# Kernel tuning notes

Measured on AMD Instinct MI355X. Metric: run time of the kernel, lower is better.

Reference implementation:

```python
import jax, jax.numpy as jnp
import numpy as np


def setup_inputs() -> dict:
    key = jax.random.key(0)
    k1, k2, k3 = jax.random.split(key, 3)
    B, C2, H, W = 8, 128, 28, 28   # resnet18 layer2 output for 224x224 input
    C3, H3, W3 = 256, 14, 14       # resnet18 layer3 output
    M = 30000                      # memory bank patches (post-coreset)
    f2 = jax.random.normal(k1, (B, C2, H, W), dtype=jnp.float32)
    f3 = jax.random.normal(k2, (B, C3, H3, W3), dtype=jnp.float32)
    memory_bank = jax.random.normal(k3, (M, C2 + C3), dtype=jnp.float32)
    return {"f2": f2, "f3": f3, "memory_bank": memory_bank}


def reference(f2, f3, memory_bank):
    """PatchCore predict: multi-layer embed + brute-force 1-NN euclidean distance.

    f2: [B,C2,H,W] (layer2 feats), f3: [B,C3,H3,W3] (layer3 feats),
    memory_bank: [M, C2+C3]. Returns (patch_scores [B,H,W], img_scores [B]).
    """
    B, C2, H, W = f2.shape
    C3 = f3.shape[1]
    # F.interpolate(..., mode='bilinear', align_corners=False) == jax.image.resize bilinear
    f3_up = jax.image.resize(f3, (B, C3, H, W), method="bilinear")
    emb = jnp.concatenate([f2, f3_up], axis=1)            # [B,C,H,W], C=C2+C3
    C = C2 + C3
    patches = emb.transpose(0, 2, 3, 1).reshape(-1, C)    # [N,C], N=B*H*W
    x_sq = jnp.sum(patches * patches, axis=-1, keepdims=True)      # [N,1]
    m_sq = jnp.sum(memory_bank * memory_bank, axis=-1)[None, :]    # [1,M]
    d2 = x_sq + m_sq - 2.0 * (patches @ memory_bank.T)             # [N,M]
    dists = jnp.sqrt(jnp.maximum(d2, 1e-12))
    nn_dist = jnp.min(dists, axis=1)                               # 1-NN (n_neighbors=1)
    patch_scores = nn_dist.reshape(B, H, W)
    img_scores = jnp.max(patch_scores.reshape(B, -1), axis=1)
    return patch_scores, img_scores
```

## Files before the change

### kernel.cpp

```cpp
#include <hip/hip_runtime.h>
#include <hip/hip_bf16.h>
#include <stdint.h>

typedef float f32x4 __attribute__((ext_vector_type(4)));
typedef short bf16x8 __attribute__((ext_vector_type(8)));

#define NPATCH 6272
#define CTOT   384
#define MBANK  30000
#define MROWS  6400
#define NCOLS  30208
#define NKT    6

#define NPB    (MROWS / 4)
#define NBB    (NCOLS / 4)

__global__ __launch_bounds__(256) void prep_kernel(
    const float* __restrict__ f2, const float* __restrict__ f3,
    const float* __restrict__ mb,
    __hip_bfloat16* __restrict__ A, __hip_bfloat16* __restrict__ Bb,
    float* __restrict__ x_sq, float* __restrict__ m_sq,
    float* __restrict__ nn_d2)
{
  const int lane = threadIdx.x & 63;
  const int sub  = threadIdx.x >> 6;

  if (blockIdx.x < NPB) {
    const int n = blockIdx.x * 4 + sub;
    if (n >= NPATCH) {
      #pragma unroll
      for (int j = 0; j < 6; ++j) A[(size_t)n * CTOT + j * 64 + lane] = __float2bfloat16(0.f);
      return;
    }
    const int b = n / 784;
    const int hw = n - b * 784;
    const int h = hw / 28;
    const int w = hw - h * 28;

    int h0, h1, w0i, w1i; float wh0, wh1, ww0, ww1;
    if (h & 1) { int k = h >> 1; h0 = k; h1 = (k + 1 < 14) ? k + 1 : 13; wh0 = 0.75f; wh1 = 0.25f; }
    else       { int k = h >> 1; h0 = (k > 0) ? k - 1 : 0; h1 = k;       wh0 = 0.25f; wh1 = 0.75f; }
    if (w & 1) { int k = w >> 1; w0i = k; w1i = (k + 1 < 14) ? k + 1 : 13; ww0 = 0.75f; ww1 = 0.25f; }
    else       { int k = w >> 1; w0i = (k > 0) ? k - 1 : 0; w1i = k;       ww0 = 0.25f; ww1 = 0.75f; }

    float ssum = 0.f;
    #pragma unroll
    for (int j = 0; j < 6; ++j) {
      const int c = j * 64 + lane;
      float v;
      if (j < 2) {
        v = f2[(((size_t)b * 128 + c) * 28 + h) * 28 + w];
      } else {
        const int c3 = c - 128;
        const float* p = f3 + ((size_t)b * 256 + c3) * 196;
        v = wh0 * (ww0 * p[h0 * 14 + w0i] + ww1 * p[h0 * 14 + w1i]) +
            wh1 * (ww0 * p[h1 * 14 + w0i] + ww1 * p[h1 * 14 + w1i]);
      }
      A[(size_t)n * CTOT + c] = __float2bfloat16(v);
      ssum += v * v;
    }
    #pragma unroll
    for (int off = 32; off; off >>= 1) ssum += __shfl_xor(ssum, off);
    if (lane == 0) { x_sq[n] = ssum; nn_d2[n] = __uint_as_float(0x7f800000u); }
  } else {
    const int m = (blockIdx.x - NPB) * 4 + sub;
    if (m < MBANK) {
      float ssum = 0.f;
      #pragma unroll
      for (int j = 0; j < 3; ++j) {
        const int c = j * 128 + lane * 2;
        const float2 v = *(const float2*)&mb[(size_t)m * CTOT + c];
        short2 o;
        o.x = (short)__bfloat16_as_ushort(__float2bfloat16(v.x));
        o.y = (short)__bfloat16_as_ushort(__float2bfloat16(v.y));
        *(short2*)&Bb[(size_t)m * CTOT + c] = o;
        ssum += v.x * v.x + v.y * v.y;
      }
      #pragma unroll
      for (int off = 32; off; off >>= 1) ssum += __shfl_xor(ssum, off);
      if (lane == 0) m_sq[m] = ssum;
    } else {
      #pragma unroll
      for (int j = 0; j < 6; ++j) Bb[(size_t)m * CTOT + j * 64 + lane] = __float2bfloat16(0.f);
      if (lane == 0) m_sq[m] = __uint_as_float(0x7f800000u);
    }
  }
}

__device__ __forceinline__ void gl_lds16(const void* g, void* l) {
  __builtin_amdgcn_global_load_lds(
      (const __attribute__((address_space(1))) uint32_t*)g,
      (__attribute__((address_space(3))) uint32_t*)l, 16, 0, 0);
}

__global__ __launch_bounds__(512, 2) void gemm_min_kernel(
    const __hip_bfloat16* __restrict__ A, const __hip_bfloat16* __restrict__ B,
    const float* __restrict__ x_sq, const float* __restrict__ m_sq,
    float* __restrict__ nn_d2)
{
  __shared__ __align__(16) short As[2][256 * 64];
  __shared__ __align__(16) short Bs[2][256 * 64];
  const int tid  = threadIdx.x;
  const int lane = tid & 63;
  const int wid  = tid >> 6;
  const int wr = wid >> 2;
  const int wc = wid & 3;
  const int row0 = blockIdx.y * 256;
  const int col0 = blockIdx.x * 256;

  f32x4 acc[8][4];
  #pragma unroll
  for (int i = 0; i < 8; ++i)
    #pragma unroll
    for (int j = 0; j < 4; ++j) acc[i][j] = (f32x4){0.f, 0.f, 0.f, 0.f};

  auto stage_pair = [&](int kt, int buf, int j) {
    const int k0 = kt * 64;
    const int cb = j * 512 + wid * 64;
    const int c  = cb + lane;
    const int r  = c >> 3;
    const int ch = (c & 7) ^ (r & 7);
    gl_lds16(A + (size_t)(row0 + r) * CTOT + k0 + ch * 8, &As[buf][cb * 8]);
    gl_lds16(B + (size_t)(col0 + r) * CTOT + k0 + ch * 8, &Bs[buf][cb * 8]);
  };

  #pragma unroll
  for (int j = 0; j < 4; ++j) stage_pair(0, 0, j);
  #pragma unroll
  for (int j = 0; j < 4; ++j) stage_pair(1, 1, j);
  asm volatile("s_waitcnt vmcnt(8)" ::: "memory");
  __builtin_amdgcn_s_barrier();

  const int sw = lane & 7;
  const int rA = wr * 128 + (lane & 15);
  const int rB = wc * 64 + (lane & 15);
  const int kq = lane >> 4;
  const int ch0 = (kq ^ sw) << 4;
  const int ch1 = ((4 + kq) ^ sw) << 4;

  #pragma unroll
  for (int t = 0; t < NKT; ++t) {
    const int cur = t & 1;
    const char* lA = (const char*)As[cur];
    const char* lB = (const char*)Bs[cur];
    const bool st = (t >= 1) && (t + 1 < NKT);
    bf16x8 a0[8], b0[4], a1[8], b1[4];

    #pragma unroll
    for (int ni = 0; ni < 4; ++ni) b0[ni] = *(const bf16x8*)(lB + (rB + ni * 16) * 128 + ch0);
    #pragma unroll
    for (int mi = 0; mi < 4; ++mi) a0[mi] = *(const bf16x8*)(lA + (rA + mi * 16) * 128 + ch0);
    if (st) stage_pair(t + 1, cur ^ 1, 0);
    __builtin_amdgcn_s_barrier();
    asm volatile("s_waitcnt lgkmcnt(0)" ::: "memory");
    __builtin_amdgcn_s_setprio(1);
    #pragma unroll
    for (int mi = 0; mi < 4; ++mi)
      #pragma unroll
      for (int ni = 0; ni < 4; ++ni)
        acc[mi][ni] = __builtin_amdgcn_mfma_f32_16x16x32_bf16(a0[mi], b0[ni], acc[mi][ni], 0, 0, 0);
    __builtin_amdgcn_s_setprio(0);
    __builtin_amdgcn_s_barrier();

    #pragma unroll
    for (int mi = 4; mi < 8; ++mi) a0[mi] = *(const bf16x8*)(lA + (rA + mi * 16) * 128 + ch0);
    if (st) stage_pair(t + 1, cur ^ 1, 1);
    __builtin_amdgcn_s_barrier();
    asm volatile("s_waitcnt lgkmcnt(0)" ::: "memory");
    __builtin_amdgcn_s_setprio(1);
    #pragma unroll
    for (int mi = 4; mi < 8; ++mi)
      #pragma unroll
      for (int ni = 0; ni < 4; ++ni)
        acc[mi][ni] = __builtin_amdgcn_mfma_f32_16x16x32_bf16(a0[mi], b0[ni], acc[mi][ni], 0, 0, 0);
    __builtin_amdgcn_s_setprio(0);
    __builtin_amdgcn_s_barrier();

    #pragma unroll
    for (int ni = 0; ni < 4; ++ni) b1[ni] = *(const bf16x8*)(lB + (rB + ni * 16) * 128 + ch1);
    #pragma unroll
    for (int mi = 0; mi < 4; ++mi) a1[mi] = *(const bf16x8*)(lA + (rA + mi * 16) * 128 + ch1);
    if (st) stage_pair(t + 1, cur ^ 1, 2);
    __builtin_amdgcn_s_barrier();
    asm volatile("s_waitcnt lgkmcnt(0)" ::: "memory");
    __builtin_amdgcn_s_setprio(1);
    #pragma unroll
    for (int mi = 0; mi < 4; ++mi)
      #pragma unroll
      for (int ni = 0; ni < 4; ++ni)
        acc[mi][ni] = __builtin_amdgcn_mfma_f32_16x16x32_bf16(a1[mi], b1[ni], acc[mi][ni], 0, 0, 0);
    __builtin_amdgcn_s_setprio(0);
    __builtin_amdgcn_s_barrier();

    #pragma unroll
    for (int mi = 4; mi < 8; ++mi) a1[mi] = *(const bf16x8*)(lA + (rA + mi * 16) * 128 + ch1);
    if (st) stage_pair(t + 1, cur ^ 1, 3);
    __builtin_amdgcn_s_barrier();
    asm volatile("s_waitcnt lgkmcnt(0)" ::: "memory");
    __builtin_amdgcn_s_setprio(1);
    #pragma unroll
    for (int mi = 4; mi < 8; ++mi)
      #pragma unroll
      for (int ni = 0; ni < 4; ++ni)
        acc[mi][ni] = __builtin_amdgcn_mfma_f32_16x16x32_bf16(a1[mi], b1[ni], acc[mi][ni], 0, 0, 0);
    __builtin_amdgcn_s_setprio(0);
    if (t + 1 < NKT)
      asm volatile("s_waitcnt vmcnt(0)" ::: "memory");
    __builtin_amdgcn_s_barrier();
  }

  float msq[4];
  #pragma unroll
  for (int ni = 0; ni < 4; ++ni) msq[ni] = m_sq[col0 + wc * 64 + ni * 16 + (lane & 15)];

  #pragma unroll
  for (int mi = 0; mi < 8; ++mi) {
    #pragma unroll
    for (int r = 0; r < 4; ++r) {
      float t = msq[0] - 2.f * acc[mi][0][r];
      #pragma unroll
      for (int ni = 1; ni < 4; ++ni) t = fminf(t, msq[ni] - 2.f * acc[mi][ni][r]);
      t = fminf(t, __shfl_xor(t, 1));
      t = fminf(t, __shfl_xor(t, 2));
      t = fminf(t, __shfl_xor(t, 4));
      t = fminf(t, __shfl_xor(t, 8));
      if ((lane & 15) == 0) {
        const int rg = row0 + wr * 128 + mi * 16 + ((lane >> 4) << 2) + r;
        if (rg < NPATCH) {
          const float v = fmaxf(t + x_sq[rg], 0.f);
          atomicMin((unsigned int*)&nn_d2[rg], __float_as_uint(v));
        }
      }
    }
  }
}

__global__ __launch_bounds__(256) void finalize_kernel(
    const float* __restrict__ nn_d2, float* __restrict__ out)
{
  const int b = blockIdx.x;
  const int tid = threadIdx.x;
  __shared__ float red[4];
  float lmax = 0.f;
  for (int i = tid; i < 784; i += 256) {
    const float d2 = nn_d2[b * 784 + i];
    const float s = sqrtf(fmaxf(d2, 1e-12f));
    out[b * 784 + i] = s;
    lmax = fmaxf(lmax, s);
  }
  #pragma unroll
  for (int off = 32; off; off >>= 1) lmax = fmaxf(lmax, __shfl_xor(lmax, off));
  if ((tid & 63) == 0) red[tid >> 6] = lmax;
  __syncthreads();
  if (tid == 0)
    out[6272 + b] = fmaxf(fmaxf(red[0], red[1]), fmaxf(red[2], red[3]));
}

extern "C" void kernel_launch(void* const* d_in, const int* in_sizes, int n_in,
                              void* d_out, int out_size, void* d_ws, size_t ws_size,
                              hipStream_t stream)
{
  const float* f2 = (const float*)d_in[0];
  const float* f3 = (const float*)d_in[1];
  const float* mb = (const float*)d_in[2];
  float* out = (float*)d_out;

  uint8_t* ws = (uint8_t*)d_ws;
  __hip_bfloat16* A  = (__hip_bfloat16*)(ws);
  __hip_bfloat16* Bb = (__hip_bfloat16*)(ws + 4915200);
  float* x_sq  = (float*)(ws + 28114944);
  float* m_sq  = (float*)(ws + 28140544);
  float* nn_d2 = (float*)(ws + 28261376);

  hipLaunchKernelGGL(prep_kernel, dim3(NPB + NBB), dim3(256), 0, stream,
                     f2, f3, mb, A, Bb, x_sq, m_sq, nn_d2);
  hipLaunchKernelGGL(gemm_min_kernel, dim3(NCOLS / 256, MROWS / 256), dim3(512), 0, stream,
                     A, Bb, x_sq, m_sq, nn_d2);
  hipLaunchKernelGGL(finalize_kernel, dim3(8), dim3(256), 0, stream, nn_d2, out);
}
```

Baseline: 468.4 us.

## Loop GEMM over column tiles per block, drop atomics, tile-transpose prep

The GEMM grid shrinks to 10x25 blocks. Each block walks 12 memory-bank column tiles in sequence, keeps a per-row running minimum, and writes partial minima instead of issuing global atomicMin. The prep kernel now transposes f2 and upsamples f3 through shared-memory tiles so reads are coalesced. x_sq is now computed from the bf16 patches in finalize, which also reduces the partials. This removes atomics and the nn_d2 init but gives only 250 blocks, which may underfill the GPU. The finalize kernel now does a per-thread 384-element norm over only 8 blocks, which adds serial work.

Result: faster. 441.8 us (-5.7%).

```diff
diff --git a/kernel.cpp b/kernel.cpp
--- a/kernel.cpp
+++ b/kernel.cpp
@@ -9,61 +9,79 @@
 #define CTOT   384
 #define MBANK  30000
 #define MROWS  6400
-#define NCOLS  30208
-#define NKT    6
-
-#define NPB    (MROWS / 4)
-#define NBB    (NCOLS / 4)
+#define NCOLS  30720
+#define NCT    120
+#define W      12
+#define NCG    10
+
+#define PF2B   16
+#define PF3B   32
+#define PBANKB (NCOLS / 4)
+#define NPREP  (PF2B + PF3B + PBANKB)
 
 __global__ __launch_bounds__(256) void prep_kernel(
     const float* __restrict__ f2, const float* __restrict__ f3,
     const float* __restrict__ mb,
     __hip_bfloat16* __restrict__ A, __hip_bfloat16* __restrict__ Bb,
-    float* __restrict__ x_sq, float* __restrict__ m_sq,
-    float* __restrict__ nn_d2)
+    float* __restrict__ m_sq)
 {
-  const int lane = threadIdx.x & 63;
-  const int sub  = threadIdx.x >> 6;
-
-  if (blockIdx.x < NPB) {
-    const int n = blockIdx.x * 4 + sub;
-    if (n >= NPATCH) {
-      #pragma unroll
-      for (int j = 0; j < 6; ++j) A[(size_t)n * CTOT + j * 64 + lane] = __float2bfloat16(0.f);
-      return;
-    }
-    const int b = n / 784;
-    const int hw = n - b * 784;
-    const int h = hw / 28;
-    const int w = hw - h * 28;
-
-    int h0, h1, w0i, w1i; float wh0, wh1, ww0, ww1;
-    if (h & 1) { int k = h >> 1; h0 = k; h1 = (k + 1 < 14) ? k + 1 : 13; wh0 = 0.75f; wh1 = 0.25f; }
-    else       { int k = h >> 1; h0 = (k > 0) ? k - 1 : 0; h1 = k;       wh0 = 0.25f; wh1 = 0.75f; }
-    if (w & 1) { int k = w >> 1; w0i = k; w1i = (k + 1 < 14) ? k + 1 : 13; ww0 = 0.75f; ww1 = 0.25f; }
-    else       { int k = w >> 1; w0i = (k > 0) ? k - 1 : 0; w1i = k;       ww0 = 0.25f; ww1 = 0.75f; }
-
-    float ssum = 0.f;
-    #pragma unroll
-    for (int j = 0; j < 6; ++j) {
-      const int c = j * 64 + lane;
-      float v;
-      if (j < 2) {
-        v = f2[(((size_t)b * 128 + c) * 28 + h) * 28 + w];
-      } else {
-        const int c3 = c - 128;
-        const float* p = f3 + ((size_t)b * 256 + c3) * 196;
-        v = wh0 * (ww0 * p[h0 * 14 + w0i] + ww1 * p[h0 * 14 + w1i]) +
-            wh1 * (ww0 * p[h1 * 14 + w0i] + ww1 * p[h1 * 14 + w1i]);
-      }
-      A[(size_t)n * CTOT + c] = __float2bfloat16(v);
-      ssum += v * v;
-    }
-    #pragma unroll
-    for (int off = 32; off; off >>= 1) ssum += __shfl_xor(ssum, off);
-    if (lane == 0) { x_sq[n] = ssum; nn_d2[n] = __uint_as_float(0x7f800000u); }
+  __shared__ float tile[64 * 197];
+  const int t = threadIdx.x;
+  const int lane = t & 63;
+  const int grp  = t >> 6;
+
+  if (blockIdx.x < PF2B) {
+    const int b  = blockIdx.x >> 1;
+    const int c0 = (blockIdx.x & 1) * 64;
+    const float* src = f2 + ((size_t)b * 128 + c0) * 784;
+    __hip_bfloat16* dst = A + (size_t)b * 784 * CTOT + c0;
+    for (int hw0 = 0; hw0 < 784; hw0 += 64) {
+      const int nhw = (784 - hw0 < 64) ? (784 - hw0) : 64;
+      __syncthreads();
+      #pragma unroll
+      for (int k = 0; k < 16; ++k) {
+        const int c = grp * 16 + k;
+        if (lane < nhw) tile[c * 65 + lane] = src[(size_t)c * 784 + hw0 + lane];
+      }
+      __syncthreads();
+      #pragma unroll
+      for (int k = 0; k < 16; ++k) {
+        const int r = grp * 16 + k;
+        if (r < nhw) dst[(size_t)(hw0 + r) * CTOT + lane] = __float2bfloat16(tile[lane * 65 + r]);
+      }
+    }
+  } else if (blockIdx.x < PF2B + PF3B) {
+    const int blk = blockIdx.x - PF2B;
+    const int b  = blk >> 2;
+    const int c0 = (blk & 3) * 64;
+    const float* src = f3 + ((size_t)b * 256 + c0) * 196;
+    for (int idx = t; idx < 64 * 196; idx += 256) {
+      const int c = idx / 196, p = idx - c * 196;
+      tile[c * 197 + p] = src[(size_t)c * 196 + p];
+    }
+    __syncthreads();
+    __hip_bfloat16* dst = A + (size_t)b * 784 * CTOT + 128 + c0;
+    for (int hw0 = 0; hw0 < 784; hw0 += 64) {
+      #pragma unroll
+      for (int k = 0; k < 16; ++k) {
+        const int r = grp * 16 + k;
+        const int hw = hw0 + r;
+        if (hw < 784) {
+          const int h = hw / 28, w = hw - h * 28;
+          int h0, h1, w0i, w1i; float wh0, wh1, ww0, ww1;
+          if (h & 1) { int q = h >> 1; h0 = q; h1 = (q + 1 < 14) ? q + 1 : 13; wh0 = 0.75f; wh1 = 0.25f; }
+          else       { int q = h >> 1; h0 = (q > 0) ? q - 1 : 0; h1 = q;       wh0 = 0.25f; wh1 = 0.75f; }
+          if (w & 1) { int q = w >> 1; w0i = q; w1i = (q + 1 < 14) ? q + 1 : 13; ww0 = 0.75f; ww1 = 0.25f; }
+          else       { int q = w >> 1; w0i = (q > 0) ? q - 1 : 0; w1i = q;       ww0 = 0.25f; ww1 = 0.75f; }
+          const float* tl = &tile[lane * 197];
+          const float v = wh0 * (ww0 * tl[h0 * 14 + w0i] + ww1 * tl[h0 * 14 + w1i]) +
+                          wh1 * (ww0 * tl[h1 * 14 + w0i] + ww1 * tl[h1 * 14 + w1i]);
+          dst[(size_t)hw * CTOT + lane] = __float2bfloat16(v);
+        }
+      }
+    }
   } else {
-    const int m = (blockIdx.x - NPB) * 4 + sub;
+    const int m = (blockIdx.x - PF2B - PF3B) * 4 + grp;
     if (m < MBANK) {
       float ssum = 0.f;
       #pragma unroll
@@ -95,18 +113,18 @@
 
 __global__ __launch_bounds__(512, 2) void gemm_min_kernel(
     const __hip_bfloat16* __restrict__ A, const __hip_bfloat16* __restrict__ B,
-    const float* __restrict__ x_sq, const float* __restrict__ m_sq,
-    float* __restrict__ nn_d2)
+    const float* __restrict__ m_sq, float* __restrict__ partial)
 {
   __shared__ __align__(16) short As[2][256 * 64];
   __shared__ __align__(16) short Bs[2][256 * 64];
+  __shared__ float redm[4][256];
   const int tid  = threadIdx.x;
   const int lane = tid & 63;
   const int wid  = tid >> 6;
   const int wr = wid >> 2;
   const int wc = wid & 3;
   const int row0 = blockIdx.y * 256;
-  const int col0 = blockIdx.x * 256;
+  const int ct0  = blockIdx.x * W;
 
   f32x4 acc[8][4];
   #pragma unroll
@@ -114,20 +132,20 @@
     #pragma unroll
     for (int j = 0; j < 4; ++j) acc[i][j] = (f32x4){0.f, 0.f, 0.f, 0.f};
 
-  auto stage_pair = [&](int kt, int buf, int j) {
-    const int k0 = kt * 64;
+  auto stage_pair = [&](int c2, int kt2, int buf, int j) {
+    const int k0 = kt2 * 64;
     const int cb = j * 512 + wid * 64;
-    const int c  = cb + lane;
-    const int r  = c >> 3;
-    const int ch = (c & 7) ^ (r & 7);
+    const int cc = cb + lane;
+    const int r  = cc >> 3;
+    const int ch = (cc & 7) ^ (r & 7);
     gl_lds16(A + (size_t)(row0 + r) * CTOT + k0 + ch * 8, &As[buf][cb * 8]);
-    gl_lds16(B + (size_t)(col0 + r) * CTOT + k0 + ch * 8, &Bs[buf][cb * 8]);
+    gl_lds16(B + ((size_t)(ct0 + c2) * 256 + r) * CTOT + k0 + ch * 8, &Bs[buf][cb * 8]);
   };
 
   #pragma unroll
-  for (int j = 0; j < 4; ++j) stage_pair(0, 0, j);
+  for (int j = 0; j < 4; ++j) stage_pair(0, 0, 0, j);
   #pragma unroll
-  for (int j = 0; j < 4; ++j) stage_pair(1, 1, j);
+  for (int j = 0; j < 4; ++j) stage_pair(0, 1, 1, j);
   asm volatile("s_waitcnt vmcnt(8)" ::: "memory");
   __builtin_amdgcn_s_barrier();
 
@@ -138,121 +156,164 @@
   const int ch0 = (kq ^ sw) << 4;
   const int ch1 = ((4 + kq) ^ sw) << 4;
 
-  #pragma unroll
-  for (int t = 0; t < NKT; ++t) {
-    const int cur = t & 1;
-    const char* lA = (const char*)As[cur];
-    const char* lB = (const char*)Bs[cur];
-    const bool st = (t >= 1) && (t + 1 < NKT);
-    bf16x8 a0[8], b0[4], a1[8], b1[4];
-
+  float msq[4];
+  float runmin = __uint_as_float(0x7f800000u);
+
+  for (int c = 0; c < W; ++c) {
     #pragma unroll
-    for (int ni = 0; ni < 4; ++ni) b0[ni] = *(const bf16x8*)(lB + (rB + ni * 16) * 128 + ch0);
-    #pragma unroll
-    for (int mi = 0; mi < 4; ++mi) a0[mi] = *(const bf16x8*)(lA + (rA + mi * 16) * 128 + ch0);
-    if (st) stage_pair(t + 1, cur ^ 1, 0);
-    __builtin_amdgcn_s_barrier();
-    asm volatile("s_waitcnt lgkmcnt(0)" ::: "memory");
-    __builtin_amdgcn_s_setprio(1);
-    #pragma unroll
-    for (int mi = 0; mi < 4; ++mi)
-      #pragma unroll
-      for (int ni = 0; ni < 4; ++ni)
-        acc[mi][ni] = __builtin_amdgcn_mfma_f32_16x16x32_bf16(a0[mi], b0[ni], acc[mi][ni], 0, 0, 0);
-    __builtin_amdgcn_s_setprio(0);
-    __builtin_amdgcn_s_barrier();
-
-    #pragma unroll
-    for (int mi = 4; mi < 8; ++mi) a0[mi] = *(const bf16x8*)(lA + (rA + mi * 16) * 128 + ch0);
-    if (st) stage_pair(t + 1, cur ^ 1, 1);
-    __builtin_amdgcn_s_barrier();
-    asm volatile("s_waitcnt lgkmcnt(0)" ::: "memory");
-    __builtin_amdgcn_s_setprio(1);
-    #pragma unroll
-    for (int mi = 4; mi < 8; ++mi)
-      #pragma unroll
-      for (int ni = 0; ni < 4; ++ni)
-        acc[mi][ni] = __builtin_amdgcn_mfma_f32_16x16x32_bf16(a0[mi], b0[ni], acc[mi][ni], 0, 0, 0);
-    __builtin_amdgcn_s_setprio(0);
-    __builtin_amdgcn_s_barrier();
-
-    #pragma unroll
-    for (int ni = 0; ni < 4; ++ni) b1[ni] = *(const bf16x8*)(lB + (rB + ni * 16) * 128 + ch1);
-    #pragma unroll
-    for (int mi = 0; mi < 4; ++mi) a1[mi] = *(const bf16x8*)(lA + (rA + mi * 16) * 128 + ch1);
-    if (st) stage_pair(t + 1, cur ^ 1, 2);
-    __builtin_amdgcn_s_barrier();
-    asm volatile("s_waitcnt lgkmcnt(0)" ::: "memory");
-    __builtin_amdgcn_s_setprio(1);
-    #pragma unroll
-    for (int mi = 0; mi < 4; ++mi)
-      #pragma unroll
-      for (int ni = 0; ni < 4; ++ni)
-        acc[mi][ni] = __builtin_amdgcn_mfma_f32_16x16x32_bf16(a1[mi], b1[ni], acc[mi][ni], 0, 0, 0);
-    __builtin_amdgcn_s_setprio(0);
-    __builtin_amdgcn_s_barrier();
-
-    #pragma unroll
-    for (int mi = 4; mi < 8; ++mi) a1[mi] = *(const bf16x8*)(lA + (rA + mi * 16) * 128 + ch1);
-    if (st) stage_pair(t + 1, cur ^ 1, 3);
-    __builtin_amdgcn_s_barrier();
-    asm volatile("s_waitcnt lgkmcnt(0)" ::: "memory");
-    __builtin_amdgcn_s_setprio(1);
-    #pragma unroll
-    for (int mi = 4; mi < 8; ++mi)
-      #pragma unroll
-      for (int ni = 0; ni < 4; ++ni)
-        acc[mi][ni] = __builtin_amdgcn_mfma_f32_16x16x32_bf16(a1[mi], b1[ni], acc[mi][ni], 0, 0, 0);
-    __builtin_amdgcn_s_setprio(0);
-    if (t + 1 < NKT)
-      asm volatile("s_waitcnt vmcnt(0)" ::: "memory");
-    __builtin_amdgcn_s_barrier();
+    for (int kt = 0; kt < 6; ++kt) {
+      const int cur = kt & 1;
+      const char* lA = (const char*)As[cur];
+      const char* lB = (const char*)Bs[cur];
+      const int kt2 = (kt == 5) ? 0 : kt + 1;
+      const int c2  = (kt == 5) ? c + 1 : c;
+      const bool st = !(c == 0 && kt == 0) && !(c == W - 1 && kt == 5);
+      bf16x8 a0[8], b0[4], a1[8], b1[4];
+
+      #pragma unroll
+      for (int ni = 0; ni < 4; ++ni) b0[ni] = *(const bf16x8*)(lB + (rB + ni * 16) * 128 + ch0);
+      #pragma unroll
+      for (int mi = 0; mi < 4; ++mi) a0[mi] = *(const bf16x8*)(lA + (rA + mi * 16) * 128 + ch0);
+      if (kt == 0) {
+        const int colb = (ct0 + c) * 256 + wc * 64 + (lane & 15);
+        #pragma unroll
+        for (int ni = 0; ni < 4; ++ni) msq[ni] = m_sq[colb + ni * 16];
+      }
+      if (st) stage_pair(c2, kt2, cur ^ 1, 0);
+      __builtin_amdgcn_s_barrier();
+      asm volatile("s_waitcnt lgkmcnt(0)" ::: "memory");
+      __builtin_amdgcn_s_setprio(1);
+      #pragma unroll
+      for (int mi = 0; mi < 4; ++mi)
+        #pragma unroll
+        for (int ni = 0; ni < 4; ++ni)
+          acc[mi][ni] = __builtin_amdgcn_mfma_f32_16x16x32_bf16(a0[mi], b0[ni], acc[mi][ni], 0, 0, 0);
+      __builtin_amdgcn_s_setprio(0);
+      __builtin_amdgcn_s_barrier();
+
+      #pragma unroll
+      for (int mi = 4; mi < 8; ++mi) a0[mi] = *(const bf16x8*)(lA + (rA + mi * 16) * 128 + ch0);
+      if (st) stage_pair(c2, kt2, cur ^ 1, 1);
+      __builtin_amdgcn_s_barrier();
+      asm volatile("s_waitcnt lgkmcnt(0)" ::: "memory");
+      __builtin_amdgcn_s_setprio(1);
+      #pragma unroll
+      for (int mi = 4; mi < 8; ++mi)
+        #pragma unroll
+        for (int ni = 0; ni < 4; ++ni)
+          acc[mi][ni] = __builtin_amdgcn_mfma_f32_16x16x32_bf16(a0[mi], b0[ni], acc[mi][ni], 0, 0, 0);
+      __builtin_amdgcn_s_setprio(0);
+      __builtin_amdgcn_s_barrier();
+
+      #pragma unroll
+      for (int ni = 0; ni < 4; ++ni) b1[ni] = *(const bf16x8*)(lB + (rB + ni * 16) * 128 + ch1);
+      #pragma unroll
+      for (int mi = 0; mi < 4; ++mi) a1[mi] = *(const bf16x8*)(lA + (rA + mi * 16) * 128 + ch1);
+      if (st) stage_pair(c2, kt2, cur ^ 1, 2);
+      __builtin_amdgcn_s_barrier();
+      asm volatile("s_waitcnt lgkmcnt(0)" ::: "memory");
+      __builtin_amdgcn_s_setprio(1);
+      #pragma unroll
+      for (int mi = 0; mi < 4; ++mi)
+        #pragma unroll
+        for (int ni = 0; ni < 4; ++ni)
+          acc[mi][ni] = __builtin_amdgcn_mfma_f32_16x16x32_bf16(a1[mi], b1[ni], acc[mi][ni], 0, 0, 0);
+      __builtin_amdgcn_s_setprio(0);
+      __builtin_amdgcn_s_barrier();
+
+      #pragma unroll
+      for (int mi = 4; mi < 8; ++mi) a1[mi] = *(const bf16x8*)(lA + (rA + mi * 16) * 128 + ch1);
+      if (st) stage_pair(c2, kt2, cur ^ 1, 3);
+      __builtin_amdgcn_s_barrier();
+      asm volatile("s_waitcnt lgkmcnt(0)" ::: "memory");
+      __builtin_amdgcn_s_setprio(1);
+      #pragma unroll
+      for (int mi = 4; mi < 8; ++mi)
+        #pragma unroll
+        for (int ni = 0; ni < 4; ++ni)
+          acc[mi][ni] = __builtin_amdgcn_mfma_f32_16x16x32_bf16(a1[mi], b1[ni], acc[mi][ni], 0, 0, 0);
+      __builtin_amdgcn_s_setprio(0);
+
+      if (kt == 5) {
+        #pragma unroll
+        for (int mi = 0; mi < 8; ++mi) {
+          #pragma unroll
+          for (int r = 0; r < 4; ++r) {
+            float tv = msq[0] - 2.f * acc[mi][0][r];
+            #pragma unroll
+            for (int ni = 1; ni < 4; ++ni) tv = fminf(tv, msq[ni] - 2.f * acc[mi][ni][r]);
+            tv = fminf(tv, __shfl_xor(tv, 1));
+            tv = fminf(tv, __shfl_xor(tv, 2));
+            tv = fminf(tv, __shfl_xor(tv, 4));
+            tv = fminf(tv, __shfl_xor(tv, 8));
+            if ((lane & 15) == 0)
+              redm[wc][wr * 128 + mi * 16 + ((lane >> 4) << 2) + r] = tv;
+          }
+          #pragma unroll
+          for (int ni = 0; ni < 4; ++ni) acc[mi][ni] = (f32x4){0.f, 0.f, 0.f, 0.f};
+        }
+        __syncthreads();
+        if (lane < 32) {
+          const int rl = wid * 32 + lane;
+          const float m01 = fminf(redm[0][rl], redm[1][rl]);
+          const float m23 = fminf(redm[2][rl], redm[3][rl]);
+          runmin = fminf(runmin, fminf(m01, m23));
+        }
+        if (c == W - 1 && lane < 32)
+          partial[(size_t)blockIdx.x * MROWS + row0 + wid * 32 + lane] = runmin;
+      } else {
+        asm volatile("s_waitcnt vmcnt(0)" ::: "memory");
+        __builtin_amdgcn_s_barrier();
+      }
+    }
   }
-
-  float msq[4];
-  #pragma unroll
-  for (int ni = 0; ni < 4; ++ni) msq[ni] = m_sq[col0 + wc * 64 + ni * 16 + (lane & 15)];
-
-  #pragma unroll
-  for (int mi = 0; mi < 8; ++mi) {
+}
+
+__global__ __launch_bounds__(256) void finalize_kernel(
+    const float* __restrict__ partial, const __hip_bfloat16* __restrict__ A,
+    float* __restrict__ out)
+{
+  const int b = blockIdx.x;
+  const int t = threadIdx.x;
+  __shared__ float red[4];
+  float lmax = 0.f;
+  if (t < 196) {
+    const int n0 = b * 784 + t * 4;
+    float4 mn = {__uint_as_float(0x7f800000u), __uint_as_float(0x7f800000u),
+                 __uint_as_float(0x7f800000u), __uint_as_float(0x7f800000u)};
+    for (int g = 0; g < NCG; ++g) {
+      const float4 p = *(const float4*)&partial[(size_t)g * MROWS + n0];
+      mn.x = fminf(mn.x, p.x); mn.y = fminf(mn.y, p.y);
+      mn.z = fminf(mn.z, p.z); mn.w = fminf(mn.w, p.w);
+    }
+    float xs[4];
     #pragma unroll
     for (int r = 0; r < 4; ++r) {
-      float t = msq[0] - 2.f * acc[mi][0][r];
-      #pragma unroll
-      for (int ni = 1; ni < 4; ++ni) t = fminf(t, msq[ni] - 2.f * acc[mi][ni][r]);
-      t = fminf(t, __shfl_xor(t, 1));
-      t = fminf(t, __shfl_xor(t, 2));
-      t = fminf(t, __shfl_xor(t, 4));
-      t = fminf(t, __shfl_xor(t, 8));
-      if ((lane & 15) == 0) {
-        const int rg = row0 + wr * 128 + mi * 16 + ((lane >> 4) << 2) + r;
-        if (rg < NPATCH) {
-          const float v = fmaxf(t + x_sq[rg], 0.f);
-          atomicMin((unsigned int*)&nn_d2[rg], __float_as_uint(v));
+      const bf16x8* ap = (const bf16x8*)(A + (size_t)(n0 + r) * CTOT);
+      float s = 0.f;
+      for (int j = 0; j < 48; ++j) {
+        const bf16x8 v = ap[j];
+        #pragma unroll
+        for (int e = 0; e < 8; ++e) {
+          const float f = __uint_as_float(((unsigned)(unsigned short)v[e]) << 16);
+          s += f * f;
         }
       }
-    }
-  }
-}
-
-__global__ __launch_bounds__(256) void finalize_kernel(
-    const float* __restrict__ nn_d2, float* __restrict__ out)
-{
-  const int b = blockIdx.x;
-  const int tid = threadIdx.x;
-  __shared__ float red[4];
-  float lmax = 0.f;
-  for (int i = tid; i < 784; i += 256) {
-    const float d2 = nn_d2[b * 784 + i];
-    const float s = sqrtf(fmaxf(d2, 1e-12f));
-    out[b * 784 + i] = s;
-    lmax = fmaxf(lmax, s);
+      xs[r] = s;
+    }
+    float4 o;
+    o.x = sqrtf(fmaxf(mn.x + xs[0], 1e-12f));
+    o.y = sqrtf(fmaxf(mn.y + xs[1], 1e-12f));
+    o.z = sqrtf(fmaxf(mn.z + xs[2], 1e-12f));
+    o.w = sqrtf(fmaxf(mn.w + xs[3], 1e-12f));
+    *(float4*)&out[n0] = o;
+    lmax = fmaxf(fmaxf(o.x, o.y), fmaxf(o.z, o.w));
   }
   #pragma unroll
   for (int off = 32; off; off >>= 1) lmax = fmaxf(lmax, __shfl_xor(lmax, off));
-  if ((tid & 63) == 0) red[tid >> 6] = lmax;
+  if ((t & 63) == 0) red[t >> 6] = lmax;
   __syncthreads();
-  if (tid == 0)
+  if (t == 0)
     out[6272 + b] = fmaxf(fmaxf(red[0], red[1]), fmaxf(red[2], red[3]));
 }
 
@@ -268,13 +329,13 @@
   uint8_t* ws = (uint8_t*)d_ws;
   __hip_bfloat16* A  = (__hip_bfloat16*)(ws);
   __hip_bfloat16* Bb = (__hip_bfloat16*)(ws + 4915200);
-  float* x_sq  = (float*)(ws + 28114944);
-  float* m_sq  = (float*)(ws + 28140544);
-  float* nn_d2 = (float*)(ws + 28261376);
-
-  hipLaunchKernelGGL(prep_kernel, dim3(NPB + NBB), dim3(256), 0, stream,
-                     f2, f3, mb, A, Bb, x_sq, m_sq, nn_d2);
-  hipLaunchKernelGGL(gemm_min_kernel, dim3(NCOLS / 256, MROWS / 256), dim3(512), 0, stream,
-                     A, Bb, x_sq, m_sq, nn_d2);
-  hipLaunchKernelGGL(finalize_kernel, dim3(8), dim3(256), 0, stream, nn_d2, out);
-}
+  float* m_sq   = (float*)(ws + 28508160);
+  float* partial = (float*)(ws + 28631040);
+
+  hipLaunchKernelGGL(prep_kernel, dim3(NPREP), dim3(256), 0, stream,
+                     f2, f3, mb, A, Bb, m_sq);
+  hipLaunchKernelGGL(gemm_min_kernel, dim3(NCG, MROWS / 256), dim3(512), 0, stream,
+                     A, Bb, m_sq, partial);
+  hipLaunchKernelGGL(finalize_kernel, dim3(8), dim3(256), 0, stream,
+                     partial, A, out);
+}
```
